# Kernel tuning notes

Hardware: AMD Instinct MI355X
Metric: run time of the kernel (lower is better)

Reference implementation:

```python
import jax, jax.numpy as jnp
import numpy as np


def setup_inputs() -> dict:
    key = jax.random.key(0)
    k1, k2 = jax.random.split(key)
    N, C, D = 16384, 4096, 1024
    x = jax.random.normal(k1, (N, D), dtype=jnp.float32)
    # torch.rand -> uniform [0, 1)
    prototype = jax.random.uniform(k2, (C, D), dtype=jnp.float32)
    return {"x": x, "prototype": prototype}


def reference(x, prototype):
    # Pairwise squared Euclidean distance:
    #   d[n, c] = sum_k (x[n, k] - p[c, k])^2
    # GEMM-based decomposition avoids the O(N*C*D) broadcast intermediate.
    x_sq = jnp.sum(x * x, axis=-1, keepdims=True)            # [N, 1]
    p_sq = jnp.sum(prototype * prototype, axis=-1)            # [C]
    cross = jnp.einsum('nd,cd->nc', x, prototype)             # [N, C] GEMM
    d = x_sq + p_sq[None, :] - 2.0 * cross                    # [N, C]
    return d
```

## Files before the change

kernel.cpp:

```cpp
#include <hip/hip_runtime.h>
#include <hip/hip_bf16.h>
#include <stdint.h>

#define NX 16384
#define NC 4096
#define DIM 1024

typedef __attribute__((ext_vector_type(8))) short bf16x8;
typedef __attribute__((ext_vector_type(4))) float f32x4;


__device__ inline unsigned short f2bf_rn(float f) {
  union { float f; unsigned u; } v; v.f = f;
  unsigned u = v.u;
  unsigned r = (u + 0x7FFFu + ((u >> 16) & 1u)) >> 16;
  return (unsigned short)r;
}

__device__ inline void gload_lds16(const void* g, const void* l) {
  __builtin_amdgcn_global_load_lds(
      (const __attribute__((address_space(1))) void*)g,
      (__attribute__((address_space(3))) void*)l,
      16, 0, 0);
}

__device__ inline f32x4 mfma_bf16_16x16x32(bf16x8 a, bf16x8 b, f32x4 c) {
  asm("v_mfma_f32_16x16x32_bf16 %0, %1, %2, %0" : "+v"(c) : "v"(a), "v"(b));
  return c;
}


__global__ __launch_bounds__(256) void convert_rows(
    const float* __restrict__ src, unsigned short* __restrict__ dst,
    float* __restrict__ sq) {
  __shared__ float red[4];
  const int row = blockIdx.x;
  const int tid = threadIdx.x;
  const size_t base = (size_t)row * DIM + tid * 4;

  const float4 v = *(const float4*)(src + base);
  float s = v.x * v.x + v.y * v.y + v.z * v.z + v.w * v.w;

  ushort4 o;
  o.x = f2bf_rn(v.x); o.y = f2bf_rn(v.y);
  o.z = f2bf_rn(v.z); o.w = f2bf_rn(v.w);
  *(ushort4*)(dst + base) = o;

  #pragma unroll
  for (int off = 32; off > 0; off >>= 1) s += __shfl_down(s, off, 64);
  const int lane = tid & 63, w = tid >> 6;
  if (lane == 0) red[w] = s;
  __syncthreads();
  if (tid == 0) sq[row] = red[0] + red[1] + red[2] + red[3];
}


#define BM 128
#define BN 128
#define BK 32

__global__ __launch_bounds__(256, 2) void dist_gemm(
    const unsigned short* __restrict__ xb,
    const unsigned short* __restrict__ pb,
    const float* __restrict__ xsq,
    const float* __restrict__ psq,
    float* __restrict__ out) {
  __shared__ short As[BM * BK];
  __shared__ short Bs[BN * BK];

  const int tid  = threadIdx.x;
  const int w    = tid >> 6;
  const int lane = tid & 63;
  const int bm = blockIdx.y * BM;
  const int bn = blockIdx.x * BN;

  const int srow = lane >> 2;
  const int skc  = (lane & 3) * 8;

  const int wr = (w >> 1) * 64;
  const int wc = (w & 1) * 64;
  const int fr = lane & 15;
  const int fk = (lane >> 4) * 8;

  f32x4 acc[4][4] = {};

  const unsigned short* gA0 = xb + (size_t)(bm + w * 16 + srow) * DIM + skc;
  const unsigned short* gA1 = xb + (size_t)(bm + (w + 4) * 16 + srow) * DIM + skc;
  const unsigned short* gB0 = pb + (size_t)(bn + w * 16 + srow) * DIM + skc;
  const unsigned short* gB1 = pb + (size_t)(bn + (w + 4) * 16 + srow) * DIM + skc;
  short* lA0 = &As[(w * 16) * BK];
  short* lA1 = &As[((w + 4) * 16) * BK];
  short* lB0 = &Bs[(w * 16) * BK];
  short* lB1 = &Bs[((w + 4) * 16) * BK];

  for (int k0 = 0; k0 < DIM; k0 += BK) {
    gload_lds16(gA0 + k0, lA0);
    gload_lds16(gA1 + k0, lA1);
    gload_lds16(gB0 + k0, lB0);
    gload_lds16(gB1 + k0, lB1);
    __syncthreads();

    bf16x8 a[4], b[4];
    #pragma unroll
    for (int i = 0; i < 4; ++i)
      a[i] = *(const bf16x8*)&As[(wr + i * 16 + fr) * BK + fk];
    #pragma unroll
    for (int j = 0; j < 4; ++j)
      b[j] = *(const bf16x8*)&Bs[(wc + j * 16 + fr) * BK + fk];

    #pragma unroll
    for (int i = 0; i < 4; ++i)
      #pragma unroll
      for (int j = 0; j < 4; ++j)
        acc[i][j] = mfma_bf16_16x16x32(a[i], b[j], acc[i][j]);

    __syncthreads();
  }

  float pv[4];
  #pragma unroll
  for (int j = 0; j < 4; ++j) pv[j] = psq[bn + wc + j * 16 + fr];

  #pragma unroll
  for (int i = 0; i < 4; ++i) {
    #pragma unroll
    for (int ri = 0; ri < 4; ++ri) {
      const int r = bm + wr + i * 16 + (lane >> 4) * 4 + ri;
      const float xv = xsq[r];
      #pragma unroll
      for (int j = 0; j < 4; ++j) {
        const int c = bn + wc + j * 16 + fr;
        out[(size_t)r * NC + c] = xv + pv[j] - 2.0f * acc[i][j][ri];
      }
    }
  }
}


extern "C" void kernel_launch(void* const* d_in, const int* in_sizes, int n_in,
                              void* d_out, int out_size, void* d_ws, size_t ws_size,
                              hipStream_t stream) {
  const float* x = (const float*)d_in[0];
  const float* p = (const float*)d_in[1];
  float* out = (float*)d_out;

  char* ws = (char*)d_ws;
  unsigned short* xb  = (unsigned short*)ws;
  unsigned short* pbb = (unsigned short*)(ws + (size_t)NX * DIM * 2);
  float* xsq = (float*)(ws + (size_t)NX * DIM * 2 + (size_t)NC * DIM * 2);
  float* psq = xsq + NX;

  convert_rows<<<NX, 256, 0, stream>>>(x, xb, xsq);
  convert_rows<<<NC, 256, 0, stream>>>(p, pbb, psq);

  dim3 grid(NC / BN, NX / BM);
  dist_gemm<<<grid, dim3(256, 1, 1), 0, stream>>>(xb, pbb, xsq, psq, out);
}
```

Measured before the change: 437.9 us.

## Rewrite distance GEMM with 256x256 tiles, double-buffered swizzled LDS, and fused conversion

Merges the two fp32-to-bf16 conversion launches into a single wave-per-row kernel. Rebuilds the GEMM with 256x256x64 block tiles and 512 threads, giving each wave an 8x4 grid of MFMA fragments. Global-to-LDS loads are double-buffered in 128 KB of dynamic LDS with an XOR swizzle, and explicit waitcnt/barriers let the next tile load overlap the current compute. It also adds s_setprio around the MFMA bursts and an XCD-aware block remap for L2 locality. The aim is more operand reuse, fewer LDS bank conflicts and hidden load latency, at the cost of higher register and LDS pressure, which can lower occupancy.

```diff
diff --git a/kernel.cpp b/kernel.cpp
--- a/kernel.cpp
+++ b/kernel.cpp
@@ -17,7 +17,7 @@
   return (unsigned short)r;
 }
 
-__device__ inline void gload_lds16(const void* g, const void* l) {
+__device__ inline void gload_lds16(const void* g, void* l) {
   __builtin_amdgcn_global_load_lds(
       (const __attribute__((address_space(1))) void*)g,
       (__attribute__((address_space(3))) void*)l,
@@ -30,108 +30,154 @@
 }
 
 
-__global__ __launch_bounds__(256) void convert_rows(
-    const float* __restrict__ src, unsigned short* __restrict__ dst,
-    float* __restrict__ sq) {
-  __shared__ float red[4];
-  const int row = blockIdx.x;
-  const int tid = threadIdx.x;
-  const size_t base = (size_t)row * DIM + tid * 4;
-
-  const float4 v = *(const float4*)(src + base);
-  float s = v.x * v.x + v.y * v.y + v.z * v.z + v.w * v.w;
-
-  ushort4 o;
-  o.x = f2bf_rn(v.x); o.y = f2bf_rn(v.y);
-  o.z = f2bf_rn(v.z); o.w = f2bf_rn(v.w);
-  *(ushort4*)(dst + base) = o;
-
-  #pragma unroll
-  for (int off = 32; off > 0; off >>= 1) s += __shfl_down(s, off, 64);
-  const int lane = tid & 63, w = tid >> 6;
-  if (lane == 0) red[w] = s;
-  __syncthreads();
-  if (tid == 0) sq[row] = red[0] + red[1] + red[2] + red[3];
-}
-
-
-#define BM 128
-#define BN 128
-#define BK 32
-
-__global__ __launch_bounds__(256, 2) void dist_gemm(
+__global__ __launch_bounds__(256) void convert_all(
+    const float* __restrict__ x, const float* __restrict__ p,
+    unsigned short* __restrict__ xb, unsigned short* __restrict__ pb,
+    float* __restrict__ xsq, float* __restrict__ psq) {
+  const int gw = blockIdx.x * 4 + (threadIdx.x >> 6);
+  const int lane = threadIdx.x & 63;
+  const float* src; unsigned short* dst; float* sq; int row;
+  if (gw < NX) { src = x; dst = xb; sq = xsq; row = gw; }
+  else         { src = p; dst = pb; sq = psq; row = gw - NX; }
+  const size_t base = (size_t)row * DIM;
+
+  float s = 0.f;
+  #pragma unroll
+  for (int j = 0; j < 4; ++j) {
+    const float4 v = *(const float4*)(src + base + j * 256 + lane * 4);
+    s += v.x * v.x + v.y * v.y + v.z * v.z + v.w * v.w;
+    ushort4 o;
+    o.x = f2bf_rn(v.x); o.y = f2bf_rn(v.y);
+    o.z = f2bf_rn(v.z); o.w = f2bf_rn(v.w);
+    *(ushort4*)(dst + base + j * 256 + lane * 4) = o;
+  }
+  #pragma unroll
+  for (int off = 32; off; off >>= 1) s += __shfl_xor(s, off, 64);
+  if (lane == 0) sq[row] = s;
+}
+
+
+#define BM 256
+#define BN 256
+#define BK 64
+#define NT (DIM / BK)
+
+__global__ __launch_bounds__(512, 2) void dist_gemm(
     const unsigned short* __restrict__ xb,
     const unsigned short* __restrict__ pb,
     const float* __restrict__ xsq,
     const float* __restrict__ psq,
     float* __restrict__ out) {
-  __shared__ short As[BM * BK];
-  __shared__ short Bs[BN * BK];
+  extern __shared__ char lds[];
 
   const int tid  = threadIdx.x;
-  const int w    = tid >> 6;
+  const int wid  = tid >> 6;
   const int lane = tid & 63;
-  const int bm = blockIdx.y * BM;
-  const int bn = blockIdx.x * BN;
-
-  const int srow = lane >> 2;
-  const int skc  = (lane & 3) * 8;
-
-  const int wr = (w >> 1) * 64;
-  const int wc = (w & 1) * 64;
-  const int fr = lane & 15;
-  const int fk = (lane >> 4) * 8;
-
-  f32x4 acc[4][4] = {};
-
-  const unsigned short* gA0 = xb + (size_t)(bm + w * 16 + srow) * DIM + skc;
-  const unsigned short* gA1 = xb + (size_t)(bm + (w + 4) * 16 + srow) * DIM + skc;
-  const unsigned short* gB0 = pb + (size_t)(bn + w * 16 + srow) * DIM + skc;
-  const unsigned short* gB1 = pb + (size_t)(bn + (w + 4) * 16 + srow) * DIM + skc;
-  short* lA0 = &As[(w * 16) * BK];
-  short* lA1 = &As[((w + 4) * 16) * BK];
-  short* lB0 = &Bs[(w * 16) * BK];
-  short* lB1 = &Bs[((w + 4) * 16) * BK];
-
-  for (int k0 = 0; k0 < DIM; k0 += BK) {
-    gload_lds16(gA0 + k0, lA0);
-    gload_lds16(gA1 + k0, lA1);
-    gload_lds16(gB0 + k0, lB0);
-    gload_lds16(gB1 + k0, lB1);
-    __syncthreads();
-
-    bf16x8 a[4], b[4];
-    #pragma unroll
-    for (int i = 0; i < 4; ++i)
-      a[i] = *(const bf16x8*)&As[(wr + i * 16 + fr) * BK + fk];
-    #pragma unroll
-    for (int j = 0; j < 4; ++j)
-      b[j] = *(const bf16x8*)&Bs[(wc + j * 16 + fr) * BK + fk];
-
-    #pragma unroll
-    for (int i = 0; i < 4; ++i)
-      #pragma unroll
-      for (int j = 0; j < 4; ++j)
-        acc[i][j] = mfma_bf16_16x16x32(a[i], b[j], acc[i][j]);
-
-    __syncthreads();
+  const int wm = wid >> 2;
+  const int wn = wid & 3;
+
+  const int bid = blockIdx.x;
+  const int xcd = bid & 7;
+  const int idx = bid >> 3;
+  const int g   = idx >> 4;
+  const int l4  = idx & 15;
+  const int tm  = xcd * 8 + (g & 1) * 4 + (l4 >> 2);
+  const int tn  = (g >> 1) * 4 + (l4 & 3);
+  const int row0 = tm * BM, col0 = tn * BN;
+
+  const int srow = wid * 8 + (lane >> 3);
+  const int scb  = ((lane & 7) ^ (lane >> 3)) << 4;
+  const char* gA = (const char*)xb + (size_t)(row0 + srow) * (DIM * 2) + scb;
+  const char* gB = (const char*)pb + (size_t)(col0 + srow) * (DIM * 2) + scb;
+
+  const int sx   = (lane & 7) << 4;
+  const int hi16 = (lane >> 4) << 4;
+  const int arow = (wm * 128 + (lane & 15)) * 128;
+  const int brow = (wn * 64  + (lane & 15)) * 128;
+  const int csw0 = (hi16 + 0)  ^ sx;
+  const int csw1 = (hi16 + 64) ^ sx;
+
+  f32x4 acc[8][4] = {};
+
+#define STAGE(kt, bufsel) do {                                               \
+    char* lA_ = lds + (bufsel) * 65536;                                      \
+    char* lB_ = lA_ + 32768;                                                 \
+    _Pragma("unroll")                                                        \
+    for (int it = 0; it < 4; ++it) {                                         \
+      gload_lds16(gA + (size_t)(kt) * 128 + (size_t)it * 64 * (DIM * 2),     \
+                  lA_ + it * 8192 + wid * 1024);                             \
+      gload_lds16(gB + (size_t)(kt) * 128 + (size_t)it * 64 * (DIM * 2),     \
+                  lB_ + it * 8192 + wid * 1024);                             \
+    }                                                                        \
+  } while (0)
+
+#define COMPUTE(bufsel) do {                                                 \
+    const char* lA_ = lds + (bufsel) * 65536;                                \
+    const char* lB_ = lA_ + 32768;                                           \
+    bf16x8 a[8], b[4];                                                       \
+    _Pragma("unroll")                                                        \
+    for (int m = 0; m < 8; ++m)                                              \
+      a[m] = *(const bf16x8*)(lA_ + arow + m * 2048 + csw0);                 \
+    _Pragma("unroll")                                                        \
+    for (int n = 0; n < 4; ++n)                                              \
+      b[n] = *(const bf16x8*)(lB_ + brow + n * 2048 + csw0);                 \
+    __builtin_amdgcn_s_setprio(1);                                           \
+    _Pragma("unroll")                                                        \
+    for (int m = 0; m < 8; ++m)                                              \
+      _Pragma("unroll")                                                      \
+      for (int n = 0; n < 4; ++n)                                            \
+        acc[m][n] = mfma_bf16_16x16x32(a[m], b[n], acc[m][n]);               \
+    __builtin_amdgcn_s_setprio(0);                                           \
+    _Pragma("unroll")                                                        \
+    for (int m = 0; m < 8; ++m)                                              \
+      a[m] = *(const bf16x8*)(lA_ + arow + m * 2048 + csw1);                 \
+    _Pragma("unroll")                                                        \
+    for (int n = 0; n < 4; ++n)                                              \
+      b[n] = *(const bf16x8*)(lB_ + brow + n * 2048 + csw1);                 \
+    __builtin_amdgcn_s_setprio(1);                                           \
+    _Pragma("unroll")                                                        \
+    for (int m = 0; m < 8; ++m)                                              \
+      _Pragma("unroll")                                                      \
+      for (int n = 0; n < 4; ++n)                                            \
+        acc[m][n] = mfma_bf16_16x16x32(a[m], b[n], acc[m][n]);               \
+    __builtin_amdgcn_s_setprio(0);                                           \
+  } while (0)
+
+  STAGE(0, 0);
+
+  #pragma unroll 2
+  for (int t = 0; t < NT - 1; ++t) {
+    STAGE(t + 1, (t + 1) & 1);
+    asm volatile("s_waitcnt vmcnt(8)" ::: "memory");
+    __builtin_amdgcn_s_barrier();
+    asm volatile("" ::: "memory");
+    COMPUTE(t & 1);
+    asm volatile("" ::: "memory");
+    __builtin_amdgcn_s_barrier();
   }
-
+  asm volatile("s_waitcnt vmcnt(0)" ::: "memory");
+  __builtin_amdgcn_s_barrier();
+  asm volatile("" ::: "memory");
+  COMPUTE((NT - 1) & 1);
+
+#undef STAGE
+#undef COMPUTE
+
+  const int orow = row0 + wm * 128 + ((lane >> 4) << 2);
+  const int ocol = col0 + wn * 64 + (lane & 15);
   float pv[4];
   #pragma unroll
-  for (int j = 0; j < 4; ++j) pv[j] = psq[bn + wc + j * 16 + fr];
-
-  #pragma unroll
-  for (int i = 0; i < 4; ++i) {
+  for (int n = 0; n < 4; ++n) pv[n] = psq[ocol + n * 16];
+
+  #pragma unroll
+  for (int m = 0; m < 8; ++m) {
     #pragma unroll
     for (int ri = 0; ri < 4; ++ri) {
-      const int r = bm + wr + i * 16 + (lane >> 4) * 4 + ri;
+      const int r = orow + m * 16 + ri;
       const float xv = xsq[r];
       #pragma unroll
-      for (int j = 0; j < 4; ++j) {
-        const int c = bn + wc + j * 16 + fr;
-        out[(size_t)r * NC + c] = xv + pv[j] - 2.0f * acc[i][j][ri];
-      }
+      for (int n = 0; n < 4; ++n)
+        out[(size_t)r * NC + ocol + n * 16] = xv + pv[n] - 2.0f * acc[m][n][ri];
     }
   }
 }
@@ -150,9 +196,13 @@
   float* xsq = (float*)(ws + (size_t)NX * DIM * 2 + (size_t)NC * DIM * 2);
   float* psq = xsq + NX;
 
-  convert_rows<<<NX, 256, 0, stream>>>(x, xb, xsq);
-  convert_rows<<<NC, 256, 0, stream>>>(p, pbb, psq);
-
-  dim3 grid(NC / BN, NX / BM);
-  dist_gemm<<<grid, dim3(256, 1, 1), 0, stream>>>(xb, pbb, xsq, psq, out);
-}
+  convert_all<<<(NX + NC) / 4, 256, 0, stream>>>(x, p, xb, pbb, xsq, psq);
+
+  static int attr_done = 0;
+  (void)hipFuncSetAttribute((const void*)dist_gemm,
+                            hipFuncAttributeMaxDynamicSharedMemorySize, 131072);
+  (void)attr_done;
+
+  dist_gemm<<<dim3((NX / BM) * (NC / BN)), dim3(512), 131072, stream>>>(
+      xb, pbb, xsq, psq, out);
+}
```

Measured after the change: 439.0 us. About the same (+0.2%).
